# Performance work log

Measured on AMD Instinct MI355X. Metric: run time of the kernel, lower is better.

The kernel has to match this reference:

```python
import jax, jax.numpy as jnp
import numpy as np

NUM_SEGMENTS = 8
EPS = 1e-5

def conv1x1(x, w, b):
    # x: [N,C,H,W], w: [O,C], b: [O]
    return jnp.einsum('nchw,oc->nohw', x, w) + b[None, :, None, None]

def maxpool2x2(x):
    n, c, h, w = x.shape
    return x.reshape(n, c, h // 2, 2, w // 2, 2).max(axis=(3, 5))

def batchnorm_train(x, gamma, beta):
    # training-mode BN over (N,H,W) per channel, biased variance (torch semantics)
    mean = x.mean(axis=(0, 2, 3), keepdims=True)
    var = x.var(axis=(0, 2, 3), keepdims=True)
    xn = (x - mean) * jax.lax.rsqrt(var + EPS)
    return xn * gamma[None, :, None, None] + beta[None, :, None, None]

def setup_inputs() -> dict:
    key = jax.random.key(0)
    ks = jax.random.split(key, 11)
    C, Ci = 512, 256
    sc_in = 1.0 / np.sqrt(C)
    sc_ci = 1.0 / np.sqrt(Ci)
    return {
        'x':     jax.random.normal(ks[0], (64, C, 28, 28), jnp.float32),
        'wg':    jax.random.normal(ks[1], (Ci, C), jnp.float32) * sc_in,
        'bg':    jax.random.normal(ks[2], (Ci,), jnp.float32) * sc_in,
        'wth':   jax.random.normal(ks[3], (Ci, C), jnp.float32) * sc_in,
        'bth':   jax.random.normal(ks[4], (Ci,), jnp.float32) * sc_in,
        'wph':   jax.random.normal(ks[5], (Ci, C), jnp.float32) * sc_in,
        'bph':   jax.random.normal(ks[6], (Ci,), jnp.float32) * sc_in,
        'wW':    jax.random.normal(ks[7], (C, Ci), jnp.float32) * sc_ci,
        'bW':    jax.random.normal(ks[8], (C,), jnp.float32) * sc_ci,
        'gamma': jax.random.normal(ks[9], (C,), jnp.float32),
        'beta':  jax.random.normal(ks[10], (C,), jnp.float32),
    }

def reference(x, wg, bg, wth, bth, wph, bph, wW, bW, gamma, beta):
    BT, C, H, W = x.shape            # [64, 512, 28, 28]
    B = BT // NUM_SEGMENTS           # 8
    Ci = wg.shape[0]                 # 256

    # projections (raw-memory reshape, matching torch .view semantics)
    g_x = maxpool2x2(conv1x1(x, wg, bg)).reshape(B, Ci, -1)      # [B, Ci, Np]
    g_x = jnp.swapaxes(g_x, 1, 2)                                 # [B, Np, Ci]
    theta = conv1x1(x, wth, bth).reshape(B, Ci, -1)               # [B, Ci, Nt]
    theta = jnp.swapaxes(theta, 1, 2)                             # [B, Nt, Ci]
    phi = maxpool2x2(conv1x1(x, wph, bph)).reshape(B, Ci, -1)     # [B, Ci, Np]

    f = jnp.einsum('btc,bcp->btp', theta, phi)                    # [B, Nt, Np]
    Np = f.shape[-1]
    y = jnp.einsum('btp,bpc->btc', f / Np, g_x)                   # [B, Nt, Ci]
    y = jnp.swapaxes(y, 1, 2).reshape(BT, -1, H, W)               # [BT, Ci, H, W]

    W_y = batchnorm_train(conv1x1(y, wW, bW), gamma, beta)        # [BT, C, H, W]
    return W_y + x
```

## Files before the change

kernel.cpp:

```cpp
#include <hip/hip_runtime.h>
#include <stdint.h>

#define BN_EPS 1e-5f

typedef float  f32x4  __attribute__((ext_vector_type(4)));
typedef short  bf16x8 __attribute__((ext_vector_type(8)));

#define MFMA16(a, b, c) __builtin_amdgcn_mfma_f32_16x16x32_bf16((a), (b), (c), 0, 0, 0)

#define GLD16(gsrc, ldst)                                                              \
    __builtin_amdgcn_global_load_lds(                                                  \
        (const __attribute__((address_space(1))) uint32_t*)(gsrc),                     \
        (__attribute__((address_space(3))) uint32_t*)(ldst), 16, 0, 0)

__device__ __forceinline__ unsigned short f2bf(float f) {
    union { float f; uint32_t u; } v; v.f = f;
    uint32_t u = v.u;
    u += 0x7FFF + ((u >> 16) & 1);
    return (unsigned short)(u >> 16);
}
__device__ __forceinline__ float bf2f(unsigned short u) {
    union { uint32_t u; float f; } v; v.u = ((uint32_t)u) << 16; return v.f;
}

__global__ __launch_bounds__(1024) void zero_kernel(float* __restrict__ p, int n) {
    int i = blockIdx.x * blockDim.x + threadIdx.x;
    if (i < n) p[i] = 0.f;
}

__global__ __launch_bounds__(256) void castw_kernel(
    const float* __restrict__ wth, const float* __restrict__ wg,
    const float* __restrict__ wph, const float* __restrict__ wW,
    unsigned short* __restrict__ wthb, unsigned short* __restrict__ wgb,
    unsigned short* __restrict__ wphb, unsigned short* __restrict__ wW2b)
{
    int i = blockIdx.x * 256 + threadIdx.x;
    if (i < 131072) wthb[i] = f2bf(wth[i]);
    else if (i < 262144) wgb[i - 131072] = f2bf(wg[i - 131072]);
    else if (i < 393216) wphb[i - 262144] = f2bf(wph[i - 262144]);
    else {
        int j = i - 393216;
        int co = j >> 8, k = j & 255;
        int q = k >> 5, a = k & 31;
        wW2b[j] = f2bf(wW[(co << 8) + (a << 3) + q]);
    }
}

__global__ __launch_bounds__(256) void castx_kernel(
    const float* __restrict__ x, unsigned short* __restrict__ xT)
{
    __shared__ float lds[64 * 65];
    const int tid = threadIdx.x;
    const int ht = blockIdx.x, ct = blockIdx.y, n = blockIdx.z;
    const int hw0 = ht << 6, ch0 = ct << 6;
    const float* xn = x + (size_t)n * 401408;
    #pragma unroll
    for (int it = 0; it < 16; ++it) {
        int idx = tid + (it << 8);
        int r = idx >> 6, cw = idx & 63;
        int hw = hw0 + cw;
        if (hw < 784) lds[r * 65 + cw] = xn[(size_t)(ch0 + r) * 784 + hw];
    }
    __syncthreads();
    #pragma unroll
    for (int it = 0; it < 8; ++it) {
        int idx = tid + (it << 8);
        int hl = idx >> 5, c2 = (idx & 31) << 1;
        int hw = hw0 + hl;
        if (hw < 784) {
            uint32_t lo = f2bf(lds[c2 * 65 + hl]);
            uint32_t hi = f2bf(lds[(c2 + 1) * 65 + hl]);
            *(uint32_t*)(xT + ((size_t)(n * 784 + hw) << 9) + ch0 + c2) = lo | (hi << 16);
        }
    }
}

__global__ __launch_bounds__(256) void proj_theta_kernel(
    const unsigned short* __restrict__ xT, const unsigned short* __restrict__ wthb,
    const float* __restrict__ bth, unsigned short* __restrict__ thetaT)
{
    __shared__ char smem[32768];
    const int tid = threadIdx.x, l = tid & 63, w = tid >> 6;
    const int jt = blockIdx.x, mb = blockIdx.y;
    const int m0 = mb << 7, j0 = jt << 7;
    const int wm = w >> 1, wn = w & 1;

    const unsigned short* srcA[2]; const unsigned short* srcB[2];
    #pragma unroll
    for (int i = 0; i < 2; ++i) {
        int c = (w << 7) + (i << 6) + l;
        int m = c & 127, kc = c >> 7;
        srcA[i] = wthb + (((size_t)(m0 + m)) << 9) + (kc << 3);
        srcB[i] = xT + (((size_t)(j0 + m)) << 9) + (kc << 3);
    }
    #pragma unroll
    for (int i = 0; i < 2; ++i) {
        GLD16(srcA[i], smem + (w << 11) + (i << 10));
        GLD16(srcB[i], smem + 8192 + (w << 11) + (i << 10));
        srcA[i] += 32; srcB[i] += 32;
    }
    f32x4 acc[4][4] = {};
    const int fr = ((l >> 4) << 7) + (l & 15);
    for (int s = 0; s < 16; ++s) {
        __syncthreads();
        char* cur = smem + ((s & 1) << 14);
        if (s + 1 < 16) {
            char* nxt = smem + (((s + 1) & 1) << 14);
            #pragma unroll
            for (int i = 0; i < 2; ++i) {
                GLD16(srcA[i], nxt + (w << 11) + (i << 10));
                GLD16(srcB[i], nxt + 8192 + (w << 11) + (i << 10));
                srcA[i] += 32; srcB[i] += 32;
            }
        }
        bf16x8 a[4], b[4];
        #pragma unroll
        for (int mf = 0; mf < 4; ++mf)
            a[mf] = *(const bf16x8*)(cur + ((fr + (wm << 6) + (mf << 4)) << 4));
        #pragma unroll
        for (int nf = 0; nf < 4; ++nf)
            b[nf] = *(const bf16x8*)(cur + 8192 + ((fr + (wn << 6) + (nf << 4)) << 4));
        #pragma unroll
        for (int mf = 0; mf < 4; ++mf)
            #pragma unroll
            for (int nf = 0; nf < 4; ++nf)
                acc[mf][nf] = MFMA16(a[mf], b[nf], acc[mf][nf]);
    }
    __syncthreads();
    unsigned short* lds16 = (unsigned short*)smem;
    #pragma unroll
    for (int mf = 0; mf < 4; ++mf) {
        int cbase = (wm << 6) + (mf << 4) + ((l >> 4) << 2);
        #pragma unroll
        for (int r = 0; r < 4; ++r) {
            float bv = bth[m0 + cbase + r];
            #pragma unroll
            for (int nf = 0; nf < 4; ++nf) {
                int jl = (wn << 6) + (nf << 4) + (l & 15);
                lds16[(cbase + r) * 128 + jl] = f2bf(acc[mf][nf][r] + bv);
            }
        }
    }
    __syncthreads();
    const int jl = tid >> 1, h = tid & 1;
    const int j = j0 + jl;
    const int n = j / 784;
    const int hw = j - n * 784;
    const int seg = n >> 3;
    unsigned short* ob = thetaT + (size_t)seg * 1605632 + ((n & 7) << 5) + (mb << 4) + (h << 3);
    #pragma unroll
    for (int q = 0; q < 8; ++q) {
        uint32_t u[8];
        #pragma unroll
        for (int e = 0; e < 8; ++e)
            u[e] = lds16[(((h << 3) + e) * 8 + q) * 128 + jl];
        uint4 pk;
        pk.x = u[0] | (u[1] << 16); pk.y = u[2] | (u[3] << 16);
        pk.z = u[4] | (u[5] << 16); pk.w = u[6] | (u[7] << 16);
        *(uint4*)(ob + (size_t)(q * 784 + hw) * 256) = pk;
    }
}

__global__ __launch_bounds__(256) void proj_gp_kernel(
    const unsigned short* __restrict__ xT,
    const unsigned short* __restrict__ wgb, const unsigned short* __restrict__ wphb,
    const float* __restrict__ bg, const float* __restrict__ bph,
    unsigned short* __restrict__ Gv, unsigned short* __restrict__ Pv)
{
    __shared__ char smem[30720];
    const int tid = threadIdx.x, l = tid & 63, w = tid >> 6;
    const int jt = blockIdx.x, mb = blockIdx.y, n = blockIdx.z;
    const int isP = mb >> 1, row0 = (mb & 1) << 7;
    const unsigned short* Wb = isP ? wphb : wgb;
    const int hw0 = jt * 112;

    const unsigned short* srcA[2]; const unsigned short* srcB[2];
    #pragma unroll
    for (int i = 0; i < 2; ++i) {
        int ca = (w << 7) + (i << 6) + l;
        srcA[i] = Wb + (((size_t)(row0 + (ca & 127))) << 9) + ((ca >> 7) << 3);
        int cb = w * 112 + (i << 6) + l;
        int jj = cb % 112, kc = cb / 112;
        srcB[i] = xT + (((size_t)(n * 784 + hw0 + jj)) << 9) + (kc << 3);
    }
    #pragma unroll
    for (int i = 0; i < 2; ++i) {
        GLD16(srcA[i], smem + (w << 11) + (i << 10));
        if (i == 0 || l < 48)
            GLD16(srcB[i], smem + 8192 + w * 1792 + (i << 10));
        srcA[i] += 32; srcB[i] += 32;
    }
    f32x4 acc[2][7] = {};
    for (int s = 0; s < 16; ++s) {
        __syncthreads();
        char* cur = smem + (s & 1) * 15360;
        if (s + 1 < 16) {
            char* nxt = smem + ((s + 1) & 1) * 15360;
            #pragma unroll
            for (int i = 0; i < 2; ++i) {
                GLD16(srcA[i], nxt + (w << 11) + (i << 10));
                if (i == 0 || l < 48)
                    GLD16(srcB[i], nxt + 8192 + w * 1792 + (i << 10));
                srcA[i] += 32; srcB[i] += 32;
            }
        }
        bf16x8 a[2], b[7];
        #pragma unroll
        for (int mf = 0; mf < 2; ++mf)
            a[mf] = *(const bf16x8*)(cur + ((((l >> 4) << 7) + (w << 5) + (mf << 4) + (l & 15)) << 4));
        #pragma unroll
        for (int nf = 0; nf < 7; ++nf)
            b[nf] = *(const bf16x8*)(cur + 8192 + ((((l >> 4) * 112) + (nf << 4) + (l & 15)) << 4));
        #pragma unroll
        for (int mf = 0; mf < 2; ++mf)
            #pragma unroll
            for (int nf = 0; nf < 7; ++nf)
                acc[mf][nf] = MFMA16(a[mf], b[nf], acc[mf][nf]);
    }
    __syncthreads();
    unsigned short* lds16 = (unsigned short*)smem;
    #pragma unroll
    for (int mf = 0; mf < 2; ++mf) {
        int cbase = (w << 5) + (mf << 4) + ((l >> 4) << 2);
        #pragma unroll
        for (int r = 0; r < 4; ++r)
            #pragma unroll
            for (int nf = 0; nf < 7; ++nf) {
                int jl = (nf << 4) + (l & 15);
                lds16[(cbase + r) * 112 + jl] = f2bf(acc[mf][nf][r]);
            }
    }
    __syncthreads();
    const int c_l = tid >> 1, ph_l = tid & 1;
    const int c = row0 + c_l;
    const float bv = (isP ? bph : bg)[c];
    const int seg = n >> 3;
    const int vr = ((n & 7) << 5) + (c >> 3);
    const int vp0 = (c & 7) * 196 + ((jt << 1) + ph_l) * 14;
    unsigned short* outp = (isP ? Pv : Gv) + (size_t)seg * 401408 + (size_t)vr * 1568 + vp0;
    const unsigned short* rowA = lds16 + c_l * 112 + ph_l * 56;
    #pragma unroll
    for (int pw = 0; pw < 14; pw += 2) {
        unsigned short o[2];
        #pragma unroll
        for (int t2 = 0; t2 < 2; ++t2) {
            int wb = (pw + t2) << 1;
            float v0 = bf2f(rowA[wb]),     v1 = bf2f(rowA[wb + 1]);
            float v2 = bf2f(rowA[wb + 28]), v3 = bf2f(rowA[wb + 29]);
            o[t2] = f2bf(fmaxf(fmaxf(v0, v1), fmaxf(v2, v3)) + bv);
        }
        *(ushort2*)(outp + pw) = make_ushort2(o[0], o[1]);
    }
}

__global__ __launch_bounds__(256) void s_kernel(
    const unsigned short* __restrict__ Gv, const unsigned short* __restrict__ Pv,
    unsigned short* __restrict__ Sb)
{
    __shared__ char smem[32768];
    const int tid = threadIdx.x, l = tid & 63, w = tid >> 6;
    const int m0 = blockIdx.x << 7, n0 = blockIdx.y << 7, seg = blockIdx.z;
    const int wm = w >> 1, wn = w & 1;
    const unsigned short* srcA[2]; const unsigned short* srcB[2];
    #pragma unroll
    for (int i = 0; i < 2; ++i) {
        int c = (w << 7) + (i << 6) + l;
        srcA[i] = Gv + (size_t)seg * 401408 + (size_t)(m0 + (c & 127)) * 1568 + ((c >> 7) << 3);
        srcB[i] = Pv + (size_t)seg * 401408 + (size_t)(n0 + (c & 127)) * 1568 + ((c >> 7) << 3);
    }
    #pragma unroll
    for (int i = 0; i < 2; ++i) {
        GLD16(srcA[i], smem + (w << 11) + (i << 10));
        GLD16(srcB[i], smem + 8192 + (w << 11) + (i << 10));
        srcA[i] += 32; srcB[i] += 32;
    }
    f32x4 acc[4][4] = {};
    const int fr = ((l >> 4) << 7) + (l & 15);
    for (int s = 0; s < 49; ++s) {
        __syncthreads();
        char* cur = smem + ((s & 1) << 14);
        if (s + 1 < 49) {
            char* nxt = smem + (((s + 1) & 1) << 14);
            #pragma unroll
            for (int i = 0; i < 2; ++i) {
                GLD16(srcA[i], nxt + (w << 11) + (i << 10));
                GLD16(srcB[i], nxt + 8192 + (w << 11) + (i << 10));
                srcA[i] += 32; srcB[i] += 32;
            }
        }
        bf16x8 a[4], b[4];
        #pragma unroll
        for (int mf = 0; mf < 4; ++mf)
            a[mf] = *(const bf16x8*)(cur + ((fr + (wm << 6) + (mf << 4)) << 4));
        #pragma unroll
        for (int nf = 0; nf < 4; ++nf)
            b[nf] = *(const bf16x8*)(cur + 8192 + ((fr + (wn << 6) + (nf << 4)) << 4));
        #pragma unroll
        for (int mf = 0; mf < 4; ++mf)
            #pragma unroll
            for (int nf = 0; nf < 4; ++nf)
                acc[mf][nf] = MFMA16(a[mf], b[nf], acc[mf][nf]);
    }
    __syncthreads();
    unsigned short* lds16 = (unsigned short*)smem;
    const float sc = 1.f / 1568.f;
    #pragma unroll
    for (int mf = 0; mf < 4; ++mf) {
        int cbase = (wm << 6) + (mf << 4) + ((l >> 4) << 2);
        #pragma unroll
        for (int r = 0; r < 4; ++r)
            #pragma unroll
            for (int nf = 0; nf < 4; ++nf) {
                int il = (wn << 6) + (nf << 4) + (l & 15);
                lds16[(cbase + r) * 128 + il] = f2bf(acc[mf][nf][r] * sc);
            }
    }
    __syncthreads();
    #pragma unroll
    for (int it = 0; it < 8; ++it) {
        int idx = tid + (it << 8);
        int crow = idx >> 4, ic = idx & 15;
        uint4 pk = *(const uint4*)(lds16 + crow * 128 + (ic << 3));
        *(uint4*)(Sb + (size_t)seg * 65536 + (size_t)(m0 + crow) * 256 + n0 + (ic << 3)) = pk;
    }
}

__global__ __launch_bounds__(256) void y_kernel(
    const unsigned short* __restrict__ Sb, const unsigned short* __restrict__ thetaT,
    unsigned short* __restrict__ YT2)
{
    __shared__ char smem[32768];
    const int tid = threadIdx.x, l = tid & 63, w = tid >> 6;
    const int jt = blockIdx.x, mt = blockIdx.y, seg = blockIdx.z;
    const int m0 = mt << 7, t0 = jt << 7;
    const int wm = w >> 1, wn = w & 1;
    const unsigned short* srcA[2]; const unsigned short* srcB[2];
    #pragma unroll
    for (int i = 0; i < 2; ++i) {
        int c = (w << 7) + (i << 6) + l;
        srcA[i] = Sb + (size_t)seg * 65536 + (size_t)(m0 + (c & 127)) * 256 + ((c >> 7) << 3);
        srcB[i] = thetaT + (size_t)seg * 1605632 + (size_t)(t0 + (c & 127)) * 256 + ((c >> 7) << 3);
    }
    #pragma unroll
    for (int i = 0; i < 2; ++i) {
        GLD16(srcA[i], smem + (w << 11) + (i << 10));
        GLD16(srcB[i], smem + 8192 + (w << 11) + (i << 10));
        srcA[i] += 32; srcB[i] += 32;
    }
    f32x4 acc[4][4] = {};
    const int fr = ((l >> 4) << 7) + (l & 15);
    for (int s = 0; s < 8; ++s) {
        __syncthreads();
        char* cur = smem + ((s & 1) << 14);
        if (s + 1 < 8) {
            char* nxt = smem + (((s + 1) & 1) << 14);
            #pragma unroll
            for (int i = 0; i < 2; ++i) {
                GLD16(srcA[i], nxt + (w << 11) + (i << 10));
                GLD16(srcB[i], nxt + 8192 + (w << 11) + (i << 10));
                srcA[i] += 32; srcB[i] += 32;
            }
        }
        bf16x8 a[4], b[4];
        #pragma unroll
        for (int mf = 0; mf < 4; ++mf)
            a[mf] = *(const bf16x8*)(cur + ((fr + (wm << 6) + (mf << 4)) << 4));
        #pragma unroll
        for (int nf = 0; nf < 4; ++nf)
            b[nf] = *(const bf16x8*)(cur + 8192 + ((fr + (wn << 6) + (nf << 4)) << 4));
        #pragma unroll
        for (int mf = 0; mf < 4; ++mf)
            #pragma unroll
            for (int nf = 0; nf < 4; ++nf)
                acc[mf][nf] = MFMA16(a[mf], b[nf], acc[mf][nf]);
    }
    __syncthreads();
    unsigned short* lds16 = (unsigned short*)smem;
    #pragma unroll
    for (int mf = 0; mf < 4; ++mf) {
        int cbase = (wm << 6) + (mf << 4) + ((l >> 4) << 2);
        #pragma unroll
        for (int r = 0; r < 4; ++r)
            #pragma unroll
            for (int nf = 0; nf < 4; ++nf) {
                int jl = (wn << 6) + (nf << 4) + (l & 15);
                lds16[(cbase + r) * 128 + jl] = f2bf(acc[mf][nf][r]);
            }
    }
    __syncthreads();
    #pragma unroll
    for (int it = 0; it < 8; ++it) {
        int idx = tid + (it << 8);
        int jl = idx >> 4, cc = idx & 15;
        uint32_t u[8];
        #pragma unroll
        for (int e = 0; e < 8; ++e)
            u[e] = lds16[((cc << 3) + e) * 128 + jl];
        uint4 pk;
        pk.x = u[0] | (u[1] << 16); pk.y = u[2] | (u[3] << 16);
        pk.z = u[4] | (u[5] << 16); pk.w = u[6] | (u[7] << 16);
        *(uint4*)(YT2 + (size_t)seg * 1605632 + (size_t)(t0 + jl) * 256 + m0 + (cc << 3)) = pk;
    }
}

__global__ __launch_bounds__(256) void zconv_kernel(
    const unsigned short* __restrict__ YT2, const unsigned short* __restrict__ wW2b,
    const float* __restrict__ bW, float* __restrict__ Z,
    float* __restrict__ sumB, float* __restrict__ sqB)
{
    __shared__ char smem[32768];
    const int tid = threadIdx.x, l = tid & 63, w = tid >> 6;
    const int jt = blockIdx.x, mt = blockIdx.y;
    const int m0 = mt << 7, j0 = jt << 7;
    const int wm = w >> 1, wn = w & 1;
    const unsigned short* srcA[2]; const unsigned short* srcB[2];
    #pragma unroll
    for (int i = 0; i < 2; ++i) {
        int c = (w << 7) + (i << 6) + l;
        int jj = c & 127, kc = c >> 7;
        srcA[i] = wW2b + (size_t)(m0 + jj) * 256 + (kc << 3);
        int j = j0 + jj;
        int nimg = j / 784;
        int hw = j - nimg * 784;
        srcB[i] = YT2 + (size_t)(nimg >> 3) * 1605632 + (size_t)hw * 256 + ((nimg & 7) << 5) + (kc << 3);
    }
    #pragma unroll
    for (int i = 0; i < 2; ++i) {
        GLD16(srcA[i], smem + (w << 11) + (i << 10));
        GLD16(srcB[i], smem + 8192 + (w << 11) + (i << 10));
        srcA[i] += 32; srcB[i] += 200704;
    }
    f32x4 acc[4][4] = {};
    const int fr = ((l >> 4) << 7) + (l & 15);
    for (int s = 0; s < 8; ++s) {
        __syncthreads();
        char* cur = smem + ((s & 1) << 14);
        if (s + 1 < 8) {
            char* nxt = smem + (((s + 1) & 1) << 14);
            #pragma unroll
            for (int i = 0; i < 2; ++i) {
                GLD16(srcA[i], nxt + (w << 11) + (i << 10));
                GLD16(srcB[i], nxt + 8192 + (w << 11) + (i << 10));
                srcA[i] += 32; srcB[i] += 200704;
            }
        }
        bf16x8 a[4], b[4];
        #pragma unroll
        for (int mf = 0; mf < 4; ++mf)
            a[mf] = *(const bf16x8*)(cur + ((fr + (wm << 6) + (mf << 4)) << 4));
        #pragma unroll
        for (int nf = 0; nf < 4; ++nf)
            b[nf] = *(const bf16x8*)(cur + 8192 + ((fr + (wn << 6) + (nf << 4)) << 4));
        #pragma unroll
        for (int mf = 0; mf < 4; ++mf)
            #pragma unroll
            for (int nf = 0; nf < 4; ++nf)
                acc[mf][nf] = MFMA16(a[mf], b[nf], acc[mf][nf]);
    }
    #pragma unroll
    for (int mf = 0; mf < 4; ++mf) {
        int co = m0 + (wm << 6) + (mf << 4) + ((l >> 4) << 2);
        float4 bv = *(const float4*)&bW[co];
        float s1[4] = {0, 0, 0, 0}, s2[4] = {0, 0, 0, 0};
        #pragma unroll
        for (int nf = 0; nf < 4; ++nf) {
            int j = j0 + (wn << 6) + (nf << 4) + (l & 15);
            float4 o;
            o.x = acc[mf][nf][0] + bv.x; o.y = acc[mf][nf][1] + bv.y;
            o.z = acc[mf][nf][2] + bv.z; o.w = acc[mf][nf][3] + bv.w;
            *(float4*)&Z[(size_t)j * 512 + co] = o;
            s1[0] += o.x; s2[0] += o.x * o.x;
            s1[1] += o.y; s2[1] += o.y * o.y;
            s1[2] += o.z; s2[2] += o.z * o.z;
            s1[3] += o.w; s2[3] += o.w * o.w;
        }
        #pragma unroll
        for (int off = 1; off < 16; off <<= 1)
            #pragma unroll
            for (int r = 0; r < 4; ++r) {
                s1[r] += __shfl_xor(s1[r], off);
                s2[r] += __shfl_xor(s2[r], off);
            }
        if ((l & 15) == 0)
            #pragma unroll
            for (int r = 0; r < 4; ++r) {
                atomicAdd(&sumB[co + r], s1[r]);
                atomicAdd(&sqB[co + r], s2[r]);
            }
    }
}

__global__ __launch_bounds__(512) void bn_finalize(
    const float* __restrict__ sumB, const float* __restrict__ sqB,
    const float* __restrict__ gamma, const float* __restrict__ beta,
    float* __restrict__ scale, float* __restrict__ shift)
{
    int c = threadIdx.x;
    if (c < 512) {
        const float invN = 1.f / 50176.f;
        float mean = sumB[c] * invN;
        float var = sqB[c] * invN - mean * mean;
        float inv = rsqrtf(var + BN_EPS);
        float sc = gamma[c] * inv;
        scale[c] = sc;
        shift[c] = beta[c] - mean * sc;
    }
}

__global__ __launch_bounds__(256) void bn_apply(
    const float* __restrict__ Z, const float* __restrict__ x,
    const float* __restrict__ scale, const float* __restrict__ shift,
    float* __restrict__ out)
{
    __shared__ float lds[128 * 65];
    const int tid = threadIdx.x;
    const int j0 = blockIdx.x << 7, co0 = blockIdx.y << 6;
    #pragma unroll
    for (int it = 0; it < 8; ++it) {
        int idx = tid + (it << 8);
        int jl = idx >> 4, c4 = (idx & 15) << 2;
        float4 v = *(const float4*)&Z[(size_t)(j0 + jl) * 512 + co0 + c4];
        lds[jl * 65 + c4] = v.x; lds[jl * 65 + c4 + 1] = v.y;
        lds[jl * 65 + c4 + 2] = v.z; lds[jl * 65 + c4 + 3] = v.w;
    }
    __syncthreads();
    #pragma unroll
    for (int it = 0; it < 8; ++it) {
        int idx = tid + (it << 8);
        int col = idx >> 5, j4 = (idx & 31) << 2;
        int j = j0 + j4;
        int n = j / 784;
        int hw = j - n * 784;
        int co = co0 + col;
        float sc = scale[co], sh = shift[co];
        size_t o = (size_t)n * 401408 + (size_t)co * 784 + hw;
        float4 xv = *(const float4*)&x[o];
        float4 r;
        r.x = fmaf(lds[(j4 + 0) * 65 + col], sc, sh) + xv.x;
        r.y = fmaf(lds[(j4 + 1) * 65 + col], sc, sh) + xv.y;
        r.z = fmaf(lds[(j4 + 2) * 65 + col], sc, sh) + xv.z;
        r.w = fmaf(lds[(j4 + 3) * 65 + col], sc, sh) + xv.w;
        *(float4*)&out[o] = r;
    }
}

extern "C" void kernel_launch(void* const* d_in, const int* in_sizes, int n_in,
                              void* d_out, int out_size, void* d_ws, size_t ws_size,
                              hipStream_t stream)
{
    const float* x     = (const float*)d_in[0];
    const float* wg    = (const float*)d_in[1];
    const float* bg    = (const float*)d_in[2];
    const float* wth   = (const float*)d_in[3];
    const float* bth   = (const float*)d_in[4];
    const float* wph   = (const float*)d_in[5];
    const float* bph   = (const float*)d_in[6];
    const float* wW    = (const float*)d_in[7];
    const float* bW    = (const float*)d_in[8];
    const float* gamma = (const float*)d_in[9];
    const float* beta  = (const float*)d_in[10];
    float* out = (float*)d_out;
    float* ws  = (float*)d_ws;

    unsigned short* xTb    = (unsigned short*)ws;
    unsigned short* YT2    = (unsigned short*)ws;
    unsigned short* thetaT = (unsigned short*)(ws + 12845056);
    unsigned short* Gv     = (unsigned short*)(ws + 19267584);
    unsigned short* Pv     = (unsigned short*)(ws + 20873216);
    unsigned short* Sb     = (unsigned short*)(ws + 22478848);
    float* Z               = ws + 12845056;
    unsigned short* wthb   = (unsigned short*)(ws + 38535168);
    unsigned short* wgb    = wthb + 131072;
    unsigned short* wphb   = wgb + 131072;
    unsigned short* wW2b   = wphb + 131072;
    float* stats           = ws + 38797312;

    zero_kernel<<<2, 1024, 0, stream>>>(stats, 2048);
    castw_kernel<<<2048, 256, 0, stream>>>(wth, wg, wph, wW, wthb, wgb, wphb, wW2b);
    castx_kernel<<<dim3(13, 8, 64), 256, 0, stream>>>(x, xTb);
    proj_theta_kernel<<<dim3(392, 2), 256, 0, stream>>>(xTb, wthb, bth, thetaT);
    proj_gp_kernel<<<dim3(7, 4, 64), 256, 0, stream>>>(xTb, wgb, wphb, bg, bph, Gv, Pv);
    s_kernel<<<dim3(2, 2, 8), 256, 0, stream>>>(Gv, Pv, Sb);
    y_kernel<<<dim3(49, 2, 8), 256, 0, stream>>>(Sb, thetaT, YT2);
    zconv_kernel<<<dim3(392, 4), 256, 0, stream>>>(YT2, wW2b, bW, Z, stats, stats + 512);
    bn_finalize<<<1, 512, 0, stream>>>(stats, stats + 512, gamma, beta,
                                       stats + 1024, stats + 1536);
    bn_apply<<<dim3(392, 8), 256, 0, stream>>>(Z, x, stats + 1024, stats + 1536, out);
}
```

Measured before the change: 626.2 us.

## Recompute output conv in BN apply instead of storing fp32 Z

The output 1x1 conv no longer writes its fp32 result Z; the first pass only accumulates per-channel sum and sum-of-squares for batch-norm statistics. A new apply kernel recomputes the bf16 GEMM tile per image, stages it through LDS, and writes the normalized result plus residual directly in NCHW layout, with the conv bias folded into the shift. This trades the Z write and reread (about 100 MB each way) for a second GEMM of the same size.

```diff
diff --git a/kernel.cpp b/kernel.cpp
--- a/kernel.cpp
+++ b/kernel.cpp
@@ -403,9 +403,9 @@
     }
 }
 
-__global__ __launch_bounds__(256) void zconv_kernel(
+__global__ __launch_bounds__(256) void zconv_stats_kernel(
     const unsigned short* __restrict__ YT2, const unsigned short* __restrict__ wW2b,
-    const float* __restrict__ bW, float* __restrict__ Z,
+    const float* __restrict__ bW,
     float* __restrict__ sumB, float* __restrict__ sqB)
 {
     __shared__ char smem[32768];
@@ -464,11 +464,9 @@
         float s1[4] = {0, 0, 0, 0}, s2[4] = {0, 0, 0, 0};
         #pragma unroll
         for (int nf = 0; nf < 4; ++nf) {
-            int j = j0 + (wn << 6) + (nf << 4) + (l & 15);
             float4 o;
             o.x = acc[mf][nf][0] + bv.x; o.y = acc[mf][nf][1] + bv.y;
             o.z = acc[mf][nf][2] + bv.z; o.w = acc[mf][nf][3] + bv.w;
-            *(float4*)&Z[(size_t)j * 512 + co] = o;
             s1[0] += o.x; s2[0] += o.x * o.x;
             s1[1] += o.y; s2[1] += o.y * o.y;
             s1[2] += o.z; s2[2] += o.z * o.z;
@@ -493,7 +491,8 @@
 __global__ __launch_bounds__(512) void bn_finalize(
     const float* __restrict__ sumB, const float* __restrict__ sqB,
     const float* __restrict__ gamma, const float* __restrict__ beta,
-    float* __restrict__ scale, float* __restrict__ shift)
+    const float* __restrict__ bW,
+    float* __restrict__ scale, float* __restrict__ shift2)
 {
     int c = threadIdx.x;
     if (c < 512) {
@@ -503,44 +502,97 @@
         float inv = rsqrtf(var + BN_EPS);
         float sc = gamma[c] * inv;
         scale[c] = sc;
-        shift[c] = beta[c] - mean * sc;
-    }
-}
-
-__global__ __launch_bounds__(256) void bn_apply(
-    const float* __restrict__ Z, const float* __restrict__ x,
-    const float* __restrict__ scale, const float* __restrict__ shift,
-    float* __restrict__ out)
-{
-    __shared__ float lds[128 * 65];
-    const int tid = threadIdx.x;
-    const int j0 = blockIdx.x << 7, co0 = blockIdx.y << 6;
-    #pragma unroll
-    for (int it = 0; it < 8; ++it) {
-        int idx = tid + (it << 8);
-        int jl = idx >> 4, c4 = (idx & 15) << 2;
-        float4 v = *(const float4*)&Z[(size_t)(j0 + jl) * 512 + co0 + c4];
-        lds[jl * 65 + c4] = v.x; lds[jl * 65 + c4 + 1] = v.y;
-        lds[jl * 65 + c4 + 2] = v.z; lds[jl * 65 + c4 + 3] = v.w;
-    }
-    __syncthreads();
-    #pragma unroll
-    for (int it = 0; it < 8; ++it) {
-        int idx = tid + (it << 8);
-        int col = idx >> 5, j4 = (idx & 31) << 2;
-        int j = j0 + j4;
-        int n = j / 784;
-        int hw = j - n * 784;
-        int co = co0 + col;
-        float sc = scale[co], sh = shift[co];
-        size_t o = (size_t)n * 401408 + (size_t)co * 784 + hw;
-        float4 xv = *(const float4*)&x[o];
-        float4 r;
-        r.x = fmaf(lds[(j4 + 0) * 65 + col], sc, sh) + xv.x;
-        r.y = fmaf(lds[(j4 + 1) * 65 + col], sc, sh) + xv.y;
-        r.z = fmaf(lds[(j4 + 2) * 65 + col], sc, sh) + xv.z;
-        r.w = fmaf(lds[(j4 + 3) * 65 + col], sc, sh) + xv.w;
-        *(float4*)&out[o] = r;
+        shift2[c] = bW[c] * sc + beta[c] - mean * sc;
+    }
+}
+
+__global__ __launch_bounds__(256) void bn_apply_kernel(
+    const unsigned short* __restrict__ YT2, const unsigned short* __restrict__ wW2b,
+    const float* __restrict__ scale, const float* __restrict__ shift2,
+    const float* __restrict__ x, float* __restrict__ out)
+{
+    __shared__ char smem[30720];
+    const int tid = threadIdx.x, l = tid & 63, w = tid >> 6;
+    const int jt = blockIdx.x, mt = blockIdx.y, n = blockIdx.z;
+    const int co0 = mt << 7;
+    const int hwb = jt * 112;
+    const size_t ybase = (size_t)(n >> 3) * 1605632 + ((n & 7) << 5);
+
+    const unsigned short* srcA[2]; const unsigned short* srcB[2];
+    #pragma unroll
+    for (int i = 0; i < 2; ++i) {
+        int ca = (w << 7) + (i << 6) + l;
+        srcA[i] = wW2b + (size_t)(co0 + (ca & 127)) * 256 + ((ca >> 7) << 3);
+        int cb = w * 112 + (i << 6) + l;
+        int jj = cb % 112, kc = cb / 112;
+        srcB[i] = YT2 + ybase + (size_t)(hwb + jj) * 256 + (kc << 3);
+    }
+    #pragma unroll
+    for (int i = 0; i < 2; ++i) {
+        GLD16(srcA[i], smem + (w << 11) + (i << 10));
+        if (i == 0 || l < 48)
+            GLD16(srcB[i], smem + 8192 + w * 1792 + (i << 10));
+        srcA[i] += 32; srcB[i] += 200704;
+    }
+    f32x4 acc[2][7] = {};
+    for (int s = 0; s < 8; ++s) {
+        __syncthreads();
+        char* cur = smem + (s & 1) * 15360;
+        if (s + 1 < 8) {
+            char* nxt = smem + ((s + 1) & 1) * 15360;
+            #pragma unroll
+            for (int i = 0; i < 2; ++i) {
+                GLD16(srcA[i], nxt + (w << 11) + (i << 10));
+                if (i == 0 || l < 48)
+                    GLD16(srcB[i], nxt + 8192 + w * 1792 + (i << 10));
+                srcA[i] += 32; srcB[i] += 200704;
+            }
+        }
+        bf16x8 a[2], b[7];
+        #pragma unroll
+        for (int mf = 0; mf < 2; ++mf)
+            a[mf] = *(const bf16x8*)(cur + ((((l >> 4) << 7) + (w << 5) + (mf << 4) + (l & 15)) << 4));
+        #pragma unroll
+        for (int nf = 0; nf < 7; ++nf)
+            b[nf] = *(const bf16x8*)(cur + 8192 + ((((l >> 4) * 112) + (nf << 4) + (l & 15)) << 4));
+        #pragma unroll
+        for (int mf = 0; mf < 2; ++mf)
+            #pragma unroll
+            for (int nf = 0; nf < 7; ++nf)
+                acc[mf][nf] = MFMA16(a[mf], b[nf], acc[mf][nf]);
+    }
+    float* ldsf = (float*)smem;
+    #pragma unroll
+    for (int h2 = 0; h2 < 2; ++h2) {
+        __syncthreads();
+        if ((w >> 1) == h2) {
+            #pragma unroll
+            for (int mf = 0; mf < 2; ++mf) {
+                int rbase = ((w & 1) << 5) + (mf << 4) + ((l >> 4) << 2);
+                #pragma unroll
+                for (int r = 0; r < 4; ++r)
+                    #pragma unroll
+                    for (int nf = 0; nf < 7; ++nf)
+                        ldsf[(rbase + r) * 116 + (nf << 4) + (l & 15)] = acc[mf][nf][r];
+            }
+        }
+        __syncthreads();
+        #pragma unroll
+        for (int it = 0; it < 7; ++it) {
+            int idx = tid + (it << 8);
+            int rl = idx / 28, jq = idx - rl * 28;
+            int co = co0 + (h2 << 6) + rl;
+            float sc = scale[co], sh = shift2[co];
+            size_t o = (size_t)n * 401408 + (size_t)co * 784 + hwb + (jq << 2);
+            float4 z = *(const float4*)&ldsf[rl * 116 + (jq << 2)];
+            float4 xv = *(const float4*)&x[o];
+            float4 rv;
+            rv.x = fmaf(z.x, sc, sh) + xv.x;
+            rv.y = fmaf(z.y, sc, sh) + xv.y;
+            rv.z = fmaf(z.z, sc, sh) + xv.z;
+            rv.w = fmaf(z.w, sc, sh) + xv.w;
+            *(float4*)&out[o] = rv;
+        }
     }
 }
 
@@ -568,7 +620,6 @@
     unsigned short* Gv     = (unsigned short*)(ws + 19267584);
     unsigned short* Pv     = (unsigned short*)(ws + 20873216);
     unsigned short* Sb     = (unsigned short*)(ws + 22478848);
-    float* Z               = ws + 12845056;
     unsigned short* wthb   = (unsigned short*)(ws + 38535168);
     unsigned short* wgb    = wthb + 131072;
     unsigned short* wphb   = wgb + 131072;
@@ -582,8 +633,9 @@
     proj_gp_kernel<<<dim3(7, 4, 64), 256, 0, stream>>>(xTb, wgb, wphb, bg, bph, Gv, Pv);
     s_kernel<<<dim3(2, 2, 8), 256, 0, stream>>>(Gv, Pv, Sb);
     y_kernel<<<dim3(49, 2, 8), 256, 0, stream>>>(Sb, thetaT, YT2);
-    zconv_kernel<<<dim3(392, 4), 256, 0, stream>>>(YT2, wW2b, bW, Z, stats, stats + 512);
-    bn_finalize<<<1, 512, 0, stream>>>(stats, stats + 512, gamma, beta,
+    zconv_stats_kernel<<<dim3(392, 4), 256, 0, stream>>>(YT2, wW2b, bW, stats, stats + 512);
+    bn_finalize<<<1, 512, 0, stream>>>(stats, stats + 512, gamma, beta, bW,
                                        stats + 1024, stats + 1536);
-    bn_apply<<<dim3(392, 8), 256, 0, stream>>>(Z, x, stats + 1024, stats + 1536, out);
-}
+    bn_apply_kernel<<<dim3(7, 4, 64), 256, 0, stream>>>(YT2, wW2b, stats + 1024,
+                                                        stats + 1536, x, out);
+}
```

Measured after the change: 622.0 us. Within noise of the previous version (-0.7%).
